# Kernel optimization log

Measured on AMD Instinct MI355X. Metric: run time of the kernel, lower is better.

The kernel has to match this reference:

```python
import jax, jax.numpy as jnp
import numpy as np

NUM_HEADS = 8
H_SCALE = 1000.0
WIND_THRESHOLD = 5.0


def setup_inputs() -> dict:
    key = jax.random.key(0)
    ks = jax.random.split(key, 8)
    B, N, C = 8, 1024, 256
    H = W = 64  # (H//2)*(W//2) == N
    x = jax.random.normal(ks[0], (B, N, C), dtype=jnp.float32)
    elevation = jax.random.uniform(ks[1], (B, N), dtype=jnp.float32)
    u_wind = jax.random.normal(ks[2], (B, H, W), dtype=jnp.float32)
    v_wind = jax.random.normal(ks[3], (B, H, W), dtype=jnp.float32)
    w_qkv = jax.random.normal(ks[4], (3 * C, C), dtype=jnp.float32) * (C ** -0.5)
    w_proj = jax.random.normal(ks[5], (C, C), dtype=jnp.float32) * (C ** -0.5)
    b_proj = jnp.zeros((C,), dtype=jnp.float32)
    alpha = jnp.float32(1.0)
    beta = jnp.float32(0.3)
    return {"x": x, "elevation": elevation, "u_wind": u_wind, "v_wind": v_wind,
            "w_qkv": w_qkv, "w_proj": w_proj, "b_proj": b_proj,
            "alpha": alpha, "beta": beta}


def _wind_strength(u_wind, v_wind):
    # 2x2 average pool of wind magnitude -> [B, N]
    B, H, W = u_wind.shape
    mag = jnp.sqrt(u_wind ** 2 + v_wind ** 2 + 1e-8)
    mag = mag.reshape(B, H // 2, 2, W // 2, 2).mean(axis=(2, 4))
    return mag.reshape(B, -1)


def _elevation_bias(elevation, u_wind, v_wind, alpha, beta):
    # elev_diff[b,i,j] = elev[b,j] - elev[b,i]
    elev_diff = elevation[:, None, :] - elevation[:, :, None]
    bias = -alpha * jax.nn.relu(elev_diff / H_SCALE)
    ws = _wind_strength(u_wind, v_wind)  # [B, N]
    wind_factor = jax.nn.sigmoid((ws[:, None, :] + ws[:, :, None]) * 0.5 - WIND_THRESHOLD)
    bias = bias * (1.0 - beta * wind_factor)
    return jnp.clip(bias, -10.0, 0.0)  # [B, N, N]


def reference(x, elevation, u_wind, v_wind, w_qkv, w_proj, b_proj, alpha, beta):
    B, N, C = x.shape
    hd = C // NUM_HEADS
    scale = hd ** -0.5
    qkv = (x @ w_qkv.T).reshape(B, N, 3, NUM_HEADS, hd)
    qkv = jnp.transpose(qkv, (2, 0, 3, 1, 4))  # [3, B, H, N, hd]
    q, k, v = qkv[0], qkv[1], qkv[2]
    scores = jnp.einsum('bhnd,bhmd->bhnm', q, k) * scale
    bias = _elevation_bias(elevation, u_wind, v_wind, alpha, beta)
    scores = scores + bias[:, None, :, :]
    attn = jax.nn.softmax(scores, axis=-1)
    out = jnp.einsum('bhnm,bhmd->bhnd', attn, v)
    out = jnp.transpose(out, (0, 2, 1, 3)).reshape(B, N, C)
    return out @ w_proj.T + b_proj
```

## Files before the change

### kernel.cpp

```cpp
#include <hip/hip_runtime.h>
#include <stdint.h>

typedef __attribute__((ext_vector_type(8))) short short8;
typedef __attribute__((ext_vector_type(8))) __bf16 bf16x8;
typedef __attribute__((ext_vector_type(4))) float f32x4;
typedef __attribute__((ext_vector_type(4))) _Float16 f16x4;
typedef __attribute__((ext_vector_type(4))) unsigned short ushort4_t;
typedef __attribute__((ext_vector_type(4))) unsigned int uint4_t;
typedef __attribute__((ext_vector_type(2))) unsigned int uint2_t;
typedef __attribute__((ext_vector_type(2))) float float2_t;

__device__ __forceinline__ unsigned short f2bf(float f) {
  unsigned int u = __builtin_bit_cast(unsigned int, f);
  u += 0x7fffu + ((u >> 16) & 1u);
  return (unsigned short)(u >> 16);
}

__device__ __forceinline__ f32x4 mfma16(short8 a, short8 b, f32x4 c) {
  return __builtin_amdgcn_mfma_f32_16x16x32_bf16(
      __builtin_bit_cast(bf16x8, a), __builtin_bit_cast(bf16x8, b), c, 0, 0, 0);
}

__device__ __forceinline__ short8 ld8(const unsigned short* p) {
  return *reinterpret_cast<const short8*>(p);
}

__global__ __launch_bounds__(256) void k_prep(const float* __restrict__ wqkv,
                                              const float* __restrict__ wproj,
                                              const float* __restrict__ u,
                                              const float* __restrict__ v,
                                              unsigned short* __restrict__ wqkv_bf,
                                              unsigned short* __restrict__ wproj_bf,
                                              float* __restrict__ ws) {
  int gx = blockIdx.x, t = threadIdx.x;
  if (gx < 768) {
    int i = gx * 256 + t;
    wqkv_bf[i] = f2bf(wqkv[i]);
  } else if (gx < 1024) {
    int i = (gx - 768) * 256 + t;
    wproj_bf[i] = f2bf(wproj[i]);
  } else {
    int i = (gx - 1024) * 256 + t;
    int b = i >> 10, n = i & 1023;
    int ph = n >> 5, pw = n & 31;
    const float* ub = u + b * 4096;
    const float* vb = v + b * 4096;
    float s = 0.f;
#pragma unroll
    for (int dy = 0; dy < 2; ++dy)
#pragma unroll
      for (int dx = 0; dx < 2; ++dx) {
        int idx = (2 * ph + dy) * 64 + (2 * pw + dx);
        float uu = ub[idx], vv = vb[idx];
        s += sqrtf(uu * uu + vv * vv + 1e-8f);
      }
    ws[i] = s * 0.25f;
  }
}

__global__ __launch_bounds__(256) void k_bias(const float* __restrict__ elev,
                                              const float* __restrict__ ws,
                                              const float* __restrict__ alphap,
                                              const float* __restrict__ betap,
                                              _Float16* __restrict__ bias16) {
  const int i = blockIdx.x, b = blockIdx.y, t = threadIdx.x;
  const float alpha = alphap[0], beta = betap[0];
  const float ei = elev[b * 1024 + i];
  const float wi = ws[b * 1024 + i];
  const int j0 = t * 4;
  f32x4 ej = *reinterpret_cast<const f32x4*>(elev + b * 1024 + j0);
  f32x4 wj = *reinterpret_cast<const f32x4*>(ws + b * 1024 + j0);
  f16x4 h;
#pragma unroll
  for (int r = 0; r < 4; ++r) {
    float dd = fmaxf((ej[r] - ei) * 1e-3f, 0.f);
    float tm = (wi + wj[r]) * 0.5f - 5.0f;
    float sig = 1.0f / (1.0f + __expf(-tm));
    float bias = -alpha * dd * (1.0f - beta * sig);
    h[r] = (_Float16)fminf(fmaxf(bias, -10.0f), 0.0f);
  }
  *reinterpret_cast<f16x4*>(bias16 + ((size_t)(b * 1024 + i)) * 1024 + j0) = h;
}

__global__ __launch_bounds__(256, 4) void k_qkv(const float* __restrict__ x,
                                                const unsigned short* __restrict__ wq_bf,
                                                unsigned short* __restrict__ qb,
                                                unsigned short* __restrict__ kb,
                                                unsigned short* __restrict__ vb) {
  __shared__ unsigned short xs[64][264];
  const int tid = threadIdx.x;
  const int w = tid >> 6, lane = tid & 63;
  const int c = lane & 15, g = lane >> 4;
  const int m0 = blockIdx.y * 64;
  const int n0 = blockIdx.x * 64;
#pragma unroll
  for (int i = 0; i < 16; ++i) {
    int idx = i * 1024 + tid * 4;
    int row = idx >> 8, col = idx & 255;
    f32x4 vv = *reinterpret_cast<const f32x4*>(x + (size_t)(m0 + row) * 256 + col);
    ushort4_t h;
#pragma unroll
    for (int j = 0; j < 4; ++j) h[j] = f2bf(vv[j]);
    *reinterpret_cast<ushort4_t*>(&xs[row][col]) = h;
  }
  __syncthreads();
  f32x4 acc[4] = {};
#pragma unroll
  for (int k0 = 0; k0 < 256; k0 += 32) {
    short8 af = ld8(&xs[w * 16 + c][k0 + g * 8]);
#pragma unroll
    for (int nb = 0; nb < 4; ++nb) {
      short8 bf = ld8(wq_bf + (size_t)(n0 + nb * 16 + c) * 256 + k0 + g * 8);
      acc[nb] = mfma16(af, bf, acc[nb]);
    }
  }
#pragma unroll
  for (int nb = 0; nb < 4; ++nb) {
    int col = n0 + nb * 16 + c;
    int s = col >> 8, rem = col & 255;
    int h = rem >> 5, d = rem & 31;
    unsigned short* dst = (s == 0) ? qb : ((s == 1) ? kb : vb);
    float scale = (s == 0) ? 0.17677669529663687f : 1.0f;
#pragma unroll
    for (int r = 0; r < 4; ++r) {
      int row = m0 + w * 16 + g * 4 + r;
      int b = row >> 10, nn = row & 1023;
      dst[((size_t)(b * 8 + h) * 1024 + nn) * 32 + d] = f2bf(acc[nb][r] * scale);
    }
  }
}

__global__ __launch_bounds__(256) void k_vtrans(const unsigned short* __restrict__ vb,
                                                unsigned short* __restrict__ vT) {
  __shared__ unsigned short tile[64][33];
  int bh = blockIdx.y;
  int n0 = blockIdx.x * 64;
  int t = threadIdx.x;
  const unsigned short* src = vb + (size_t)bh * 1024 * 32 + (size_t)n0 * 32;
  short8 vv = ld8(src + t * 8);
  int n = (t * 8) >> 5, d0 = (t * 8) & 31;
#pragma unroll
  for (int j = 0; j < 8; ++j) tile[n][d0 + j] = (unsigned short)vv[j];
  __syncthreads();
  unsigned short* dst = vT + (size_t)bh * 32 * 1024;
  int d = (t * 8) >> 6, nn0 = (t * 8) & 63;
  short8 o;
#pragma unroll
  for (int j = 0; j < 8; ++j) o[j] = (short)tile[nn0 + j][d];
  *reinterpret_cast<short8*>(dst + (size_t)d * 1024 + n0 + nn0) = o;
}

__global__ __launch_bounds__(256, 4) void k_attn(const unsigned short* __restrict__ qb,
                                                 const unsigned short* __restrict__ kb,
                                                 const unsigned short* __restrict__ vT,
                                                 const _Float16* __restrict__ bias16,
                                                 float* __restrict__ o_part,
                                                 float* __restrict__ ml_part) {
  __shared__ _Float16 bias_lds[2][32][72];
  __shared__ unsigned short p_lds[4][32][72];
  const int tid = threadIdx.x;
  const int w = tid >> 6, lane = tid & 63;
  const int c = lane & 15, g = lane >> 4;
  const int q0 = blockIdx.x * 32, b = blockIdx.y;
  const int hg = blockIdx.z & 1, sp = blockIdx.z >> 1;
  const int h = hg * 4 + w;
  const size_t bh = (size_t)(b * 8 + h);
  const int kvbase = sp * 512;

  short8 qf[2];
#pragma unroll
  for (int qs = 0; qs < 2; ++qs)
    qf[qs] = ld8(qb + (bh * 1024 + q0 + qs * 16 + c) * 32 + g * 8);

  f32x4 oacc[2][2] = {};
  float mold[2] = {-1e30f, -1e30f};
  float lrow[2] = {0.f, 0.f};

  const int sqr = tid >> 3, skv = (tid & 7) * 8;
  const _Float16* bg = bias16 + ((size_t)(b * 1024 + q0 + sqr)) * 1024;
  *reinterpret_cast<uint4_t*>(&bias_lds[0][sqr][skv]) =
      *reinterpret_cast<const uint4_t*>(bg + kvbase + skv);
  __syncthreads();

  for (int t8 = 0; t8 < 8; ++t8) {
    const int buf = t8 & 1;
    const int kv0 = kvbase + t8 * 64;
    uint4_t vpre;
    if (t8 < 7) vpre = *reinterpret_cast<const uint4_t*>(bg + kv0 + 64 + skv);

    short8 kf[4];
#pragma unroll
    for (int t = 0; t < 4; ++t)
      kf[t] = ld8(kb + (bh * 1024 + kv0 + t * 16 + c) * 32 + g * 8);

#pragma unroll
    for (int qs = 0; qs < 2; ++qs) {
      f32x4 z = {};
      f32x4 s[4];
#pragma unroll
      for (int t = 0; t < 4; ++t) s[t] = mfma16(kf[t], qf[qs], z);
      float p[4][4];
      float m16 = -1e30f;
#pragma unroll
      for (int t = 0; t < 4; ++t) {
        f16x4 bv = *reinterpret_cast<const f16x4*>(&bias_lds[buf][qs * 16 + c][t * 16 + 4 * g]);
#pragma unroll
        for (int r = 0; r < 4; ++r) {
          float sv = s[t][r] + (float)bv[r];
          p[t][r] = sv;
          m16 = fmaxf(m16, sv);
        }
      }
      m16 = fmaxf(m16, __shfl_xor(m16, 16));
      m16 = fmaxf(m16, __shfl_xor(m16, 32));
      float mn = fmaxf(mold[qs], m16);
      float corr = __expf(mold[qs] - mn);
      mold[qs] = mn;
      float ps = 0.f;
#pragma unroll
      for (int t = 0; t < 4; ++t)
#pragma unroll
        for (int r = 0; r < 4; ++r) {
          float e = __expf(p[t][r] - mn);
          p[t][r] = e;
          ps += e;
        }
      ps += __shfl_xor(ps, 16);
      ps += __shfl_xor(ps, 32);
      lrow[qs] = lrow[qs] * corr + ps;
#pragma unroll
      for (int hs = 0; hs < 2; ++hs) oacc[qs][hs] *= corr;
#pragma unroll
      for (int t = 0; t < 4; ++t) {
        uint2_t pk;
        pk[0] = (unsigned)f2bf(p[t][0]) | ((unsigned)f2bf(p[t][1]) << 16);
        pk[1] = (unsigned)f2bf(p[t][2]) | ((unsigned)f2bf(p[t][3]) << 16);
        *reinterpret_cast<uint2_t*>(&p_lds[w][qs * 16 + c][t * 16 + 4 * g]) = pk;
      }
    }

#pragma unroll
    for (int t2 = 0; t2 < 2; ++t2) {
      short8 pf[2];
#pragma unroll
      for (int qs = 0; qs < 2; ++qs)
        pf[qs] = ld8(&p_lds[w][qs * 16 + c][t2 * 32 + g * 8]);
#pragma unroll
      for (int hs = 0; hs < 2; ++hs) {
        short8 vf = ld8(vT + (bh * 32 + hs * 16 + c) * 1024 + kv0 + t2 * 32 + g * 8);
#pragma unroll
        for (int qs = 0; qs < 2; ++qs)
          oacc[qs][hs] = mfma16(vf, pf[qs], oacc[qs][hs]);
      }
    }

    if (t8 < 7) *reinterpret_cast<uint4_t*>(&bias_lds[buf ^ 1][sqr][skv]) = vpre;
    __syncthreads();
  }

#pragma unroll
  for (int qs = 0; qs < 2; ++qs) {
    size_t qrow = ((size_t)sp * 64 + bh) * 1024 + q0 + qs * 16 + c;
#pragma unroll
    for (int hs = 0; hs < 2; ++hs)
      *reinterpret_cast<f32x4*>(o_part + qrow * 32 + hs * 16 + 4 * g) = oacc[qs][hs];
    if (g == 0) {
      float2_t ml = {mold[qs], lrow[qs]};
      *reinterpret_cast<float2_t*>(ml_part + qrow * 2) = ml;
    }
  }
}

__global__ __launch_bounds__(256) void k_combine(const float* __restrict__ o_part,
                                                 const float* __restrict__ ml_part,
                                                 float* __restrict__ ao) {
  const int id = blockIdx.x * 256 + threadIdx.x;
  const int d4 = id & 7;
  const int q = (id >> 3) & 1023;
  const int bh = id >> 13;
  const size_t r0 = ((size_t)bh * 1024 + q);
  const size_t r1 = ((size_t)64 * 1024) + r0;
  f32x4 o0 = *reinterpret_cast<const f32x4*>(o_part + r0 * 32 + d4 * 4);
  f32x4 o1 = *reinterpret_cast<const f32x4*>(o_part + r1 * 32 + d4 * 4);
  float m0 = ml_part[r0 * 2], l0 = ml_part[r0 * 2 + 1];
  float m1 = ml_part[r1 * 2], l1 = ml_part[r1 * 2 + 1];
  float mm = fmaxf(m0, m1);
  float a0 = __expf(m0 - mm), a1 = __expf(m1 - mm);
  float inv = 1.0f / (a0 * l0 + a1 * l1);
  f32x4 res = (o0 * a0 + o1 * a1) * inv;
  int b = bh >> 3, h = bh & 7;
  *reinterpret_cast<f32x4*>(ao + ((size_t)(b * 1024 + q)) * 256 + h * 32 + d4 * 4) = res;
}

__global__ __launch_bounds__(256, 4) void k_proj(const float* __restrict__ ao,
                                                 const unsigned short* __restrict__ wp_bf,
                                                 const float* __restrict__ bproj,
                                                 float* __restrict__ out) {
  __shared__ unsigned short xs[64][264];
  const int tid = threadIdx.x;
  const int w = tid >> 6, lane = tid & 63;
  const int c = lane & 15, g = lane >> 4;
  const int m0 = blockIdx.y * 64;
  const int n0 = blockIdx.x * 64;
#pragma unroll
  for (int i = 0; i < 16; ++i) {
    int idx = i * 1024 + tid * 4;
    int row = idx >> 8, col = idx & 255;
    f32x4 vv = *reinterpret_cast<const f32x4*>(ao + (size_t)(m0 + row) * 256 + col);
    ushort4_t hh;
#pragma unroll
    for (int j = 0; j < 4; ++j) hh[j] = f2bf(vv[j]);
    *reinterpret_cast<ushort4_t*>(&xs[row][col]) = hh;
  }
  __syncthreads();
  f32x4 acc[4] = {};
#pragma unroll
  for (int k0 = 0; k0 < 256; k0 += 32) {
    short8 af = ld8(&xs[w * 16 + c][k0 + g * 8]);
#pragma unroll
    for (int nb = 0; nb < 4; ++nb) {
      short8 bf = ld8(wp_bf + (size_t)(n0 + nb * 16 + c) * 256 + k0 + g * 8);
      acc[nb] = mfma16(af, bf, acc[nb]);
    }
  }
#pragma unroll
  for (int nb = 0; nb < 4; ++nb) {
    int col = n0 + nb * 16 + c;
    float bv = bproj[col];
#pragma unroll
    for (int r = 0; r < 4; ++r) {
      int row = m0 + w * 16 + g * 4 + r;
      out[(size_t)row * 256 + col] = acc[nb][r] + bv;
    }
  }
}

extern "C" void kernel_launch(void* const* d_in, const int* in_sizes, int n_in,
                              void* d_out, int out_size, void* d_ws, size_t ws_size,
                              hipStream_t stream) {
  const float* x = (const float*)d_in[0];
  const float* elev = (const float*)d_in[1];
  const float* uw = (const float*)d_in[2];
  const float* vw = (const float*)d_in[3];
  const float* wqkv = (const float*)d_in[4];
  const float* wproj = (const float*)d_in[5];
  const float* bproj = (const float*)d_in[6];
  const float* alpha = (const float*)d_in[7];
  const float* beta = (const float*)d_in[8];
  float* out = (float*)d_out;

  char* p = (char*)d_ws;
  auto alloc = [&](size_t bytes) {
    char* r = p;
    p += (bytes + 255) & ~(size_t)255;
    return r;
  };
  float* ws_wind = (float*)alloc(8192 * 4);
  unsigned short* wqkv_bf = (unsigned short*)alloc((size_t)768 * 256 * 2);
  unsigned short* wproj_bf = (unsigned short*)alloc((size_t)256 * 256 * 2);
  unsigned short* qb = (unsigned short*)alloc((size_t)2097152 * 2);
  unsigned short* kb = (unsigned short*)alloc((size_t)2097152 * 2);
  unsigned short* vb = (unsigned short*)alloc((size_t)2097152 * 2);
  unsigned short* vT = (unsigned short*)alloc((size_t)2097152 * 2);
  _Float16* bias16 = (_Float16*)alloc((size_t)8 * 1024 * 1024 * 2);
  float* o_part = (float*)alloc((size_t)2 * 2097152 * 4);
  float* ml_part = (float*)alloc((size_t)2 * 65536 * 2 * 4);
  float* ao = (float*)alloc((size_t)2097152 * 4);

  k_prep<<<dim3(1056), dim3(256), 0, stream>>>(wqkv, wproj, uw, vw, wqkv_bf, wproj_bf, ws_wind);
  k_bias<<<dim3(1024, 8), dim3(256), 0, stream>>>(elev, ws_wind, alpha, beta, bias16);
  k_qkv<<<dim3(12, 128), dim3(256), 0, stream>>>(x, wqkv_bf, qb, kb, vb);
  k_vtrans<<<dim3(16, 64), dim3(256), 0, stream>>>(vb, vT);
  k_attn<<<dim3(32, 8, 4), dim3(256), 0, stream>>>(qb, kb, vT, bias16, o_part, ml_part);
  k_combine<<<dim3(2048), dim3(256), 0, stream>>>(o_part, ml_part, ao);
  k_proj<<<dim3(4, 128), dim3(256), 0, stream>>>(ao, wproj_bf, bproj, out);
}
```

Baseline: 169.2 us.

## Fuse bias into attention, V transpose into QKV GEMM, combine into projection

Removes the separate bias, V-transpose and split-KV combine kernels. The elevation/wind bias tile is now computed on the fly inside the attention loop from per-row elevation and wind vectors, so the 16 MB fp16 bias matrix is never written or read. The QKV GEMM widens each block to 192 output columns and writes V already transposed. The projection kernel merges the two split-KV partials before its GEMM. This cuts kernel launches and global memory traffic, at the cost of extra exp and arithmetic inside attention and fewer, larger blocks for the QKV and projection GEMMs.

New measurement: 162.8 us. 3.8% less time.

```diff
diff --git a/kernel.cpp b/kernel.cpp
--- a/kernel.cpp
+++ b/kernel.cpp
@@ -6,7 +6,6 @@
 typedef __attribute__((ext_vector_type(4))) float f32x4;
 typedef __attribute__((ext_vector_type(4))) _Float16 f16x4;
 typedef __attribute__((ext_vector_type(4))) unsigned short ushort4_t;
-typedef __attribute__((ext_vector_type(4))) unsigned int uint4_t;
 typedef __attribute__((ext_vector_type(2))) unsigned int uint2_t;
 typedef __attribute__((ext_vector_type(2))) float float2_t;
 
@@ -58,102 +57,68 @@
   }
 }
 
-__global__ __launch_bounds__(256) void k_bias(const float* __restrict__ elev,
-                                              const float* __restrict__ ws,
-                                              const float* __restrict__ alphap,
-                                              const float* __restrict__ betap,
-                                              _Float16* __restrict__ bias16) {
-  const int i = blockIdx.x, b = blockIdx.y, t = threadIdx.x;
-  const float alpha = alphap[0], beta = betap[0];
-  const float ei = elev[b * 1024 + i];
-  const float wi = ws[b * 1024 + i];
-  const int j0 = t * 4;
-  f32x4 ej = *reinterpret_cast<const f32x4*>(elev + b * 1024 + j0);
-  f32x4 wj = *reinterpret_cast<const f32x4*>(ws + b * 1024 + j0);
-  f16x4 h;
-#pragma unroll
-  for (int r = 0; r < 4; ++r) {
-    float dd = fmaxf((ej[r] - ei) * 1e-3f, 0.f);
-    float tm = (wi + wj[r]) * 0.5f - 5.0f;
-    float sig = 1.0f / (1.0f + __expf(-tm));
-    float bias = -alpha * dd * (1.0f - beta * sig);
-    h[r] = (_Float16)fminf(fmaxf(bias, -10.0f), 0.0f);
-  }
-  *reinterpret_cast<f16x4*>(bias16 + ((size_t)(b * 1024 + i)) * 1024 + j0) = h;
-}
-
 __global__ __launch_bounds__(256, 4) void k_qkv(const float* __restrict__ x,
                                                 const unsigned short* __restrict__ wq_bf,
                                                 unsigned short* __restrict__ qb,
                                                 unsigned short* __restrict__ kb,
-                                                unsigned short* __restrict__ vb) {
+                                                unsigned short* __restrict__ vT) {
   __shared__ unsigned short xs[64][264];
   const int tid = threadIdx.x;
   const int w = tid >> 6, lane = tid & 63;
   const int c = lane & 15, g = lane >> 4;
   const int m0 = blockIdx.y * 64;
-  const int n0 = blockIdx.x * 64;
+  const int n0 = blockIdx.x * 192;
 #pragma unroll
   for (int i = 0; i < 16; ++i) {
     int idx = i * 1024 + tid * 4;
     int row = idx >> 8, col = idx & 255;
     f32x4 vv = *reinterpret_cast<const f32x4*>(x + (size_t)(m0 + row) * 256 + col);
-    ushort4_t h;
-#pragma unroll
-    for (int j = 0; j < 4; ++j) h[j] = f2bf(vv[j]);
-    *reinterpret_cast<ushort4_t*>(&xs[row][col]) = h;
+    ushort4_t hh;
+#pragma unroll
+    for (int j = 0; j < 4; ++j) hh[j] = f2bf(vv[j]);
+    *reinterpret_cast<ushort4_t*>(&xs[row][col]) = hh;
   }
   __syncthreads();
-  f32x4 acc[4] = {};
+  f32x4 acc[12] = {};
 #pragma unroll
   for (int k0 = 0; k0 < 256; k0 += 32) {
     short8 af = ld8(&xs[w * 16 + c][k0 + g * 8]);
 #pragma unroll
-    for (int nb = 0; nb < 4; ++nb) {
+    for (int nb = 0; nb < 12; ++nb) {
       short8 bf = ld8(wq_bf + (size_t)(n0 + nb * 16 + c) * 256 + k0 + g * 8);
       acc[nb] = mfma16(af, bf, acc[nb]);
     }
   }
 #pragma unroll
-  for (int nb = 0; nb < 4; ++nb) {
+  for (int nb = 0; nb < 12; ++nb) {
     int col = n0 + nb * 16 + c;
     int s = col >> 8, rem = col & 255;
     int h = rem >> 5, d = rem & 31;
-    unsigned short* dst = (s == 0) ? qb : ((s == 1) ? kb : vb);
-    float scale = (s == 0) ? 0.17677669529663687f : 1.0f;
-#pragma unroll
-    for (int r = 0; r < 4; ++r) {
-      int row = m0 + w * 16 + g * 4 + r;
-      int b = row >> 10, nn = row & 1023;
-      dst[((size_t)(b * 8 + h) * 1024 + nn) * 32 + d] = f2bf(acc[nb][r] * scale);
-    }
-  }
-}
-
-__global__ __launch_bounds__(256) void k_vtrans(const unsigned short* __restrict__ vb,
-                                                unsigned short* __restrict__ vT) {
-  __shared__ unsigned short tile[64][33];
-  int bh = blockIdx.y;
-  int n0 = blockIdx.x * 64;
-  int t = threadIdx.x;
-  const unsigned short* src = vb + (size_t)bh * 1024 * 32 + (size_t)n0 * 32;
-  short8 vv = ld8(src + t * 8);
-  int n = (t * 8) >> 5, d0 = (t * 8) & 31;
-#pragma unroll
-  for (int j = 0; j < 8; ++j) tile[n][d0 + j] = (unsigned short)vv[j];
-  __syncthreads();
-  unsigned short* dst = vT + (size_t)bh * 32 * 1024;
-  int d = (t * 8) >> 6, nn0 = (t * 8) & 63;
-  short8 o;
-#pragma unroll
-  for (int j = 0; j < 8; ++j) o[j] = (short)tile[nn0 + j][d];
-  *reinterpret_cast<short8*>(dst + (size_t)d * 1024 + n0 + nn0) = o;
+    int nrow0 = m0 + w * 16 + g * 4;
+    int b = nrow0 >> 10, nn = nrow0 & 1023;
+    size_t bh = (size_t)(b * 8 + h);
+    if (s == 2) {
+      ushort4_t pk;
+#pragma unroll
+      for (int r = 0; r < 4; ++r) pk[r] = f2bf(acc[nb][r]);
+      *reinterpret_cast<ushort4_t*>(vT + (bh * 32 + d) * 1024 + nn) = pk;
+    } else {
+      unsigned short* dst = (s == 0) ? qb : kb;
+      float scale = (s == 0) ? 0.17677669529663687f : 1.0f;
+#pragma unroll
+      for (int r = 0; r < 4; ++r)
+        dst[(bh * 1024 + nn + r) * 32 + d] = f2bf(acc[nb][r] * scale);
+    }
+  }
 }
 
 __global__ __launch_bounds__(256, 4) void k_attn(const unsigned short* __restrict__ qb,
                                                  const unsigned short* __restrict__ kb,
                                                  const unsigned short* __restrict__ vT,
-                                                 const _Float16* __restrict__ bias16,
+                                                 const float* __restrict__ elev,
+                                                 const float* __restrict__ wsd,
+                                                 const float* __restrict__ alphap,
+                                                 const float* __restrict__ betap,
                                                  float* __restrict__ o_part,
                                                  float* __restrict__ ml_part) {
   __shared__ _Float16 bias_lds[2][32][72];
@@ -166,6 +131,33 @@
   const int h = hg * 4 + w;
   const size_t bh = (size_t)(b * 8 + h);
   const int kvbase = sp * 512;
+  const float alpha = alphap[0], beta = betap[0];
+
+  const int sqr = tid >> 3, skv = (tid & 7) * 8;
+  const float* eb = elev + b * 1024;
+  const float* wb = wsd + b * 1024;
+  const float ei = eb[q0 + sqr], wi = wb[q0 + sqr];
+
+  auto stage_bias = [&](int buf, int kv0) {
+    f32x4 ej0 = *reinterpret_cast<const f32x4*>(eb + kv0 + skv);
+    f32x4 ej1 = *reinterpret_cast<const f32x4*>(eb + kv0 + skv + 4);
+    f32x4 wj0 = *reinterpret_cast<const f32x4*>(wb + kv0 + skv);
+    f32x4 wj1 = *reinterpret_cast<const f32x4*>(wb + kv0 + skv + 4);
+    f16x4 h0, h1;
+#pragma unroll
+    for (int j = 0; j < 4; ++j) {
+      float dd = fmaxf((ej0[j] - ei) * 1e-3f, 0.f);
+      float sig = 1.0f / (1.0f + __expf(5.0f - (wi + wj0[j]) * 0.5f));
+      h0[j] = (_Float16)fminf(fmaxf(-alpha * dd * (1.0f - beta * sig), -10.0f), 0.0f);
+      float dd1 = fmaxf((ej1[j] - ei) * 1e-3f, 0.f);
+      float sig1 = 1.0f / (1.0f + __expf(5.0f - (wi + wj1[j]) * 0.5f));
+      h1[j] = (_Float16)fminf(fmaxf(-alpha * dd1 * (1.0f - beta * sig1), -10.0f), 0.0f);
+    }
+    *reinterpret_cast<f16x4*>(&bias_lds[buf][sqr][skv]) = h0;
+    *reinterpret_cast<f16x4*>(&bias_lds[buf][sqr][skv + 4]) = h1;
+  };
+
+  stage_bias(0, kvbase);
 
   short8 qf[2];
 #pragma unroll
@@ -175,18 +167,11 @@
   f32x4 oacc[2][2] = {};
   float mold[2] = {-1e30f, -1e30f};
   float lrow[2] = {0.f, 0.f};
-
-  const int sqr = tid >> 3, skv = (tid & 7) * 8;
-  const _Float16* bg = bias16 + ((size_t)(b * 1024 + q0 + sqr)) * 1024;
-  *reinterpret_cast<uint4_t*>(&bias_lds[0][sqr][skv]) =
-      *reinterpret_cast<const uint4_t*>(bg + kvbase + skv);
   __syncthreads();
 
   for (int t8 = 0; t8 < 8; ++t8) {
     const int buf = t8 & 1;
     const int kv0 = kvbase + t8 * 64;
-    uint4_t vpre;
-    if (t8 < 7) vpre = *reinterpret_cast<const uint4_t*>(bg + kv0 + 64 + skv);
 
     short8 kf[4];
 #pragma unroll
@@ -254,7 +239,7 @@
       }
     }
 
-    if (t8 < 7) *reinterpret_cast<uint4_t*>(&bias_lds[buf ^ 1][sqr][skv]) = vpre;
+    if (t8 < 7) stage_bias(buf ^ 1, kv0 + 64);
     __syncthreads();
   }
 
@@ -271,65 +256,55 @@
   }
 }
 
-__global__ __launch_bounds__(256) void k_combine(const float* __restrict__ o_part,
+__global__ __launch_bounds__(256, 2) void k_proj(const float* __restrict__ o_part,
                                                  const float* __restrict__ ml_part,
-                                                 float* __restrict__ ao) {
-  const int id = blockIdx.x * 256 + threadIdx.x;
-  const int d4 = id & 7;
-  const int q = (id >> 3) & 1023;
-  const int bh = id >> 13;
-  const size_t r0 = ((size_t)bh * 1024 + q);
-  const size_t r1 = ((size_t)64 * 1024) + r0;
-  f32x4 o0 = *reinterpret_cast<const f32x4*>(o_part + r0 * 32 + d4 * 4);
-  f32x4 o1 = *reinterpret_cast<const f32x4*>(o_part + r1 * 32 + d4 * 4);
-  float m0 = ml_part[r0 * 2], l0 = ml_part[r0 * 2 + 1];
-  float m1 = ml_part[r1 * 2], l1 = ml_part[r1 * 2 + 1];
-  float mm = fmaxf(m0, m1);
-  float a0 = __expf(m0 - mm), a1 = __expf(m1 - mm);
-  float inv = 1.0f / (a0 * l0 + a1 * l1);
-  f32x4 res = (o0 * a0 + o1 * a1) * inv;
-  int b = bh >> 3, h = bh & 7;
-  *reinterpret_cast<f32x4*>(ao + ((size_t)(b * 1024 + q)) * 256 + h * 32 + d4 * 4) = res;
-}
-
-__global__ __launch_bounds__(256, 4) void k_proj(const float* __restrict__ ao,
                                                  const unsigned short* __restrict__ wp_bf,
                                                  const float* __restrict__ bproj,
                                                  float* __restrict__ out) {
-  __shared__ unsigned short xs[64][264];
+  __shared__ unsigned short xs[32][264];
   const int tid = threadIdx.x;
   const int w = tid >> 6, lane = tid & 63;
   const int c = lane & 15, g = lane >> 4;
-  const int m0 = blockIdx.y * 64;
-  const int n0 = blockIdx.x * 64;
-#pragma unroll
-  for (int i = 0; i < 16; ++i) {
-    int idx = i * 1024 + tid * 4;
-    int row = idx >> 8, col = idx & 255;
-    f32x4 vv = *reinterpret_cast<const f32x4*>(ao + (size_t)(m0 + row) * 256 + col);
+  const int wm = w & 1, wn = w >> 1;
+  const int m0 = blockIdx.x * 32;
+  const int b = m0 >> 10, q0 = m0 & 1023;
+
+  const int qq = tid >> 3, d0 = (tid & 7) * 4;
+#pragma unroll
+  for (int h = 0; h < 8; ++h) {
+    size_t r0 = ((size_t)(b * 8 + h) * 1024 + q0 + qq);
+    size_t r1 = r0 + (size_t)64 * 1024;
+    f32x4 o0 = *reinterpret_cast<const f32x4*>(o_part + r0 * 32 + d0);
+    f32x4 o1 = *reinterpret_cast<const f32x4*>(o_part + r1 * 32 + d0);
+    float2_t ml0 = *reinterpret_cast<const float2_t*>(ml_part + r0 * 2);
+    float2_t ml1 = *reinterpret_cast<const float2_t*>(ml_part + r1 * 2);
+    float mm = fmaxf(ml0[0], ml1[0]);
+    float a0 = __expf(ml0[0] - mm), a1 = __expf(ml1[0] - mm);
+    float inv = 1.0f / (a0 * ml0[1] + a1 * ml1[1]);
     ushort4_t hh;
 #pragma unroll
-    for (int j = 0; j < 4; ++j) hh[j] = f2bf(vv[j]);
-    *reinterpret_cast<ushort4_t*>(&xs[row][col]) = hh;
+    for (int j = 0; j < 4; ++j) hh[j] = f2bf((o0[j] * a0 + o1[j] * a1) * inv);
+    *reinterpret_cast<ushort4_t*>(&xs[qq][h * 32 + d0]) = hh;
   }
   __syncthreads();
-  f32x4 acc[4] = {};
+
+  f32x4 acc[8] = {};
 #pragma unroll
   for (int k0 = 0; k0 < 256; k0 += 32) {
-    short8 af = ld8(&xs[w * 16 + c][k0 + g * 8]);
-#pragma unroll
-    for (int nb = 0; nb < 4; ++nb) {
-      short8 bf = ld8(wp_bf + (size_t)(n0 + nb * 16 + c) * 256 + k0 + g * 8);
+    short8 af = ld8(&xs[wm * 16 + c][k0 + g * 8]);
+#pragma unroll
+    for (int nb = 0; nb < 8; ++nb) {
+      short8 bf = ld8(wp_bf + (size_t)(wn * 128 + nb * 16 + c) * 256 + k0 + g * 8);
       acc[nb] = mfma16(af, bf, acc[nb]);
     }
   }
 #pragma unroll
-  for (int nb = 0; nb < 4; ++nb) {
-    int col = n0 + nb * 16 + c;
+  for (int nb = 0; nb < 8; ++nb) {
+    int col = wn * 128 + nb * 16 + c;
     float bv = bproj[col];
 #pragma unroll
     for (int r = 0; r < 4; ++r) {
-      int row = m0 + w * 16 + g * 4 + r;
+      int row = m0 + wm * 16 + g * 4 + r;
       out[(size_t)row * 256 + col] = acc[nb][r] + bv;
     }
   }
@@ -360,18 +335,12 @@
   unsigned short* wproj_bf = (unsigned short*)alloc((size_t)256 * 256 * 2);
   unsigned short* qb = (unsigned short*)alloc((size_t)2097152 * 2);
   unsigned short* kb = (unsigned short*)alloc((size_t)2097152 * 2);
-  unsigned short* vb = (unsigned short*)alloc((size_t)2097152 * 2);
   unsigned short* vT = (unsigned short*)alloc((size_t)2097152 * 2);
-  _Float16* bias16 = (_Float16*)alloc((size_t)8 * 1024 * 1024 * 2);
   float* o_part = (float*)alloc((size_t)2 * 2097152 * 4);
   float* ml_part = (float*)alloc((size_t)2 * 65536 * 2 * 4);
-  float* ao = (float*)alloc((size_t)2097152 * 4);
 
   k_prep<<<dim3(1056), dim3(256), 0, stream>>>(wqkv, wproj, uw, vw, wqkv_bf, wproj_bf, ws_wind);
-  k_bias<<<dim3(1024, 8), dim3(256), 0, stream>>>(elev, ws_wind, alpha, beta, bias16);
-  k_qkv<<<dim3(12, 128), dim3(256), 0, stream>>>(x, wqkv_bf, qb, kb, vb);
-  k_vtrans<<<dim3(16, 64), dim3(256), 0, stream>>>(vb, vT);
-  k_attn<<<dim3(32, 8, 4), dim3(256), 0, stream>>>(qb, kb, vT, bias16, o_part, ml_part);
-  k_combine<<<dim3(2048), dim3(256), 0, stream>>>(o_part, ml_part, ao);
-  k_proj<<<dim3(4, 128), dim3(256), 0, stream>>>(ao, wproj_bf, bproj, out);
-}
+  k_qkv<<<dim3(4, 128), dim3(256), 0, stream>>>(x, wqkv_bf, qb, kb, vT);
+  k_attn<<<dim3(32, 8, 4), dim3(256), 0, stream>>>(qb, kb, vT, elev, ws_wind, alpha, beta, o_part, ml_part);
+  k_proj<<<dim3(256), dim3(256), 0, stream>>>(o_part, ml_part, wproj_bf, bproj, out);
+}
```
